# Kernel tuning notes

Hardware: AMD Instinct MI355X
Metric: run time of the kernel (lower is better)

## Reference

```python
import jax, jax.numpy as jnp
import numpy as np

S, B, C = 7, 2, 20
LC, LN = 5.0, 0.5  # lambda_coord, lambda_noobj
CELL = 1.0 / S


def _iou(b1, b2):
    # center (x, y, w, h) boxes, broadcastable [..., 4]
    x1a, y1a = b1[..., 0] - b1[..., 2] / 2, b1[..., 1] - b1[..., 3] / 2
    x2a, y2a = b1[..., 0] + b1[..., 2] / 2, b1[..., 1] + b1[..., 3] / 2
    x1b, y1b = b2[..., 0] - b2[..., 2] / 2, b2[..., 1] - b2[..., 3] / 2
    x2b, y2b = b2[..., 0] + b2[..., 2] / 2, b2[..., 1] + b2[..., 3] / 2
    iw = jnp.maximum(jnp.minimum(x2a, x2b) - jnp.maximum(x1a, x1b), 0.0)
    ih = jnp.maximum(jnp.minimum(y2a, y2b) - jnp.maximum(y1a, y1b), 0.0)
    inter = iw * ih
    union = b1[..., 2] * b1[..., 3] + b2[..., 2] * b2[..., 3] - inter
    return inter / jnp.maximum(union, 1e-10)


def setup_inputs() -> dict:
    key = jax.random.key(0)
    k1, k2, k3 = jax.random.split(key, 3)
    N, T = 16384, 16
    outputs = jax.random.normal(k1, (N, S, S, B * 5 + C), dtype=jnp.float32)
    # normalized xywh, kept strictly inside (0,1) so grid indices are valid
    boxes = jax.random.uniform(k2, (N, T, 4), dtype=jnp.float32, minval=0.01, maxval=0.99)
    labels = jax.random.randint(k3, (N, T), 1, C + 1)  # class labels in 1..C
    return {"outputs": outputs, "boxes": boxes, "labels": labels}


def reference(outputs, boxes, labels):
    N = outputs.shape[0]
    T = boxes.shape[1]
    bbox = outputs[..., : B * 5].reshape(N, S, S, B, 5)
    conf = bbox[..., 4]                         # [N,S,S,B]
    cls_logits = outputs[..., B * 5:]           # [N,S,S,C]
    # decode predicted centers to absolute image coords (as in the original)
    gx = jnp.arange(S, dtype=outputs.dtype)[None, :, None]  # column index
    gy = jnp.arange(S, dtype=outputs.dtype)[:, None, None]  # row index
    px = (bbox[..., 0] + gx) * CELL
    py = (bbox[..., 1] + gy) * CELL
    pred = jnp.stack([px, py, bbox[..., 2], bbox[..., 3]], axis=-1)  # [N,S,S,B,4]

    tx, ty, tw, th = boxes[..., 0], boxes[..., 1], boxes[..., 2], boxes[..., 3]  # [N,T]
    gxi = (tx * S).astype(jnp.int32)
    gyi = (ty * S).astype(jnp.int32)
    offx = tx * S - gxi.astype(tx.dtype)
    offy = ty * S - gyi.astype(ty.dtype)

    bi = jnp.arange(N)[:, None]  # [N,1] broadcasts with [N,T]
    cell_pred = pred[bi, gyi, gxi]          # [N,T,B,4]
    cell_conf = conf[bi, gyi, gxi]          # [N,T,B]
    cell_cls = cls_logits[bi, gyi, gxi]     # [N,T,C]

    ious = _iou(boxes[:, :, None, :], cell_pred)   # [N,T,B]
    best = (B - 1) - jnp.argmax(ious[..., ::-1], axis=-1)  # [N,T]

    bp = jnp.take_along_axis(cell_pred, best[:, :, None, None], axis=2)[:, :, 0, :]  # [N,T,4]
    bconf = jnp.take_along_axis(cell_conf, best[:, :, None], axis=2)[:, :, 0]        # [N,T]

    eps = 1e-6
    box_loss = (
        (bp[..., 0] - offx) ** 2
        + (bp[..., 1] - offy) ** 2
        + (jnp.sqrt(jnp.maximum(bp[..., 2], eps)) - jnp.sqrt(jnp.maximum(tw, eps))) ** 2
        + (jnp.sqrt(jnp.maximum(bp[..., 3], eps)) - jnp.sqrt(jnp.maximum(th, eps))) ** 2
    ).sum(axis=-1)                                     # [N]
    obj_loss = ((bconf - 1.0) ** 2).sum(axis=-1)        # [N]

    probs = jax.nn.softmax(cell_cls, axis=-1)           # [N,T,C]
    onehot = jax.nn.one_hot(labels - 1, C, dtype=probs.dtype)
    class_loss = ((probs - onehot) ** 2).sum(axis=-1).sum(axis=-1)  # [N]

    obj_mask = jnp.zeros((N, S, S, B), dtype=bool).at[bi, gyi, gxi, best].set(True)
    nm = ~obj_mask
    cnt = nm.sum(axis=(1, 2, 3)).astype(conf.dtype)     # always > 0 (T < S*S*B)
    noobj_loss = (conf ** 2 * nm).sum(axis=(1, 2, 3)) / cnt  # mean over unmasked conf

    per_img = LC * box_loss + class_loss + obj_loss + LN * noobj_loss
    return per_img.mean()
```

## Files before the change

kernel.cpp:

```cpp
#include <hip/hip_runtime.h>

#define Cnum 20
#define NCH  30
#define NCONF 98
#define IMGF 1470
#define LCf 5.0f
#define LNf 0.5f

__global__ __launch_bounds__(256) void yolo_loss_kernel(
    const float* __restrict__ outputs,
    const float* __restrict__ boxes,
    const int*   __restrict__ labels,
    float*       __restrict__ per_img)
{
    const int tid  = threadIdx.x;
    const int wave = tid >> 6;
    const int lane = tid & 63;
    const int n    = blockIdx.x * 4 + wave;
    const int t    = lane >> 2;
    const int q    = lane & 3;

    const float* img = outputs + (size_t)n * IMGF;

    const float4 bx = reinterpret_cast<const float4*>(boxes)[(size_t)n * 16 + t];
    const int   lab = labels[(size_t)n * 16 + t] - 1;

    const float tx = bx.x, ty = bx.y, tw = bx.z, th = bx.w;
    const float fx = tx * 7.0f, fy = ty * 7.0f;
    const int gxi = (int)fx, gyi = (int)fy;
    const float offx = fx - (float)gxi;
    const float offy = fy - (float)gyi;
    const int cellIdx = gyi * 7 + gxi;
    const float* cell = img + cellIdx * NCH;

    float ns;
    {
        int c = lane >> 1, b = lane & 1;
        float cf = img[c * NCH + b * 5 + 4];
        ns = cf * cf;
        if (lane < NCONF - 64) {
            int s2 = lane + 64;
            int c2 = s2 >> 1, b2 = s2 & 1;
            float cf2 = img[c2 * NCH + b2 * 5 + 4];
            ns += cf2 * cf2;
        }
    }

    float f[8] = {0.f, 0.f, 0.f, 0.f, 0.f, 0.f, 0.f, 0.f};
    if (q == 0) {
        #pragma unroll
        for (int i = 0; i < 8; ++i) f[i] = cell[i];
    } else if (q == 1) {
        f[0] = cell[8];
        f[1] = cell[9];
    }
    const float e5 = __shfl_xor(f[5], 1);
    const float e6 = __shfl_xor(f[6], 1);
    const float e7 = __shfl_xor(f[7], 1);

    float px = 0.f, py = 0.f, pw = 0.f, ph = 0.f, pc = 0.f, iou_own = 0.f;
    if (q < 2) {
        float rx = (q == 0) ? f[0] : e5;
        float ry = (q == 0) ? f[1] : e6;
        pw       = (q == 0) ? f[2] : e7;
        ph       = (q == 0) ? f[3] : f[0];
        pc       = (q == 0) ? f[4] : f[1];
        px = (rx + (float)gxi) * (1.0f / 7.0f);
        py = (ry + (float)gyi) * (1.0f / 7.0f);

        float x1a = tx - tw * 0.5f, y1a = ty - th * 0.5f;
        float x2a = tx + tw * 0.5f, y2a = ty + th * 0.5f;
        float x1b = px - pw * 0.5f, y1b = py - ph * 0.5f;
        float x2b = px + pw * 0.5f, y2b = py + ph * 0.5f;
        float iw = fmaxf(fminf(x2a, x2b) - fmaxf(x1a, x1b), 0.0f);
        float ih = fmaxf(fminf(y2a, y2b) - fmaxf(y1a, y1b), 0.0f);
        float inter = iw * ih;
        float uni = tw * th + pw * ph - inter;
        iou_own = inter / fmaxf(uni, 1e-10f);
    }
    const float iou_other = __shfl_xor(iou_own, 1);
    int bestq = 0;
    if (q < 2) {
        float i0 = (q == 0) ? iou_own   : iou_other;
        float i1 = (q == 0) ? iou_other : iou_own;
        bestq = (i1 >= i0) ? 1 : 0;
    }
    const int best = __shfl(bestq, lane & ~3);
    const int s = cellIdx * 2 + best;

    float contrib = 0.0f;
    const float eps = 1e-6f;
    if (q == best) {
        float dx = px - offx, dy = py - offy;
        float dw = sqrtf(fmaxf(pw, eps)) - sqrtf(fmaxf(tw, eps));
        float dh = sqrtf(fmaxf(ph, eps)) - sqrtf(fmaxf(th, eps));
        float box_l = dx * dx + dy * dy + dw * dw + dh * dh;
        float obj_l = (pc - 1.0f) * (pc - 1.0f);
        contrib = LCf * box_l + obj_l;
    }

    bool firstv = true;
    #pragma unroll
    for (int j = 0; j < 15; ++j) {
        int sj = __shfl(s, 4 * j);
        if (j < t && sj == s) firstv = false;
    }
    float ms = 0.0f, mc = 0.0f;
    if (q == best && firstv) { ms = pc * pc; mc = 1.0f; }

    {
        float cv[5];
        #pragma unroll
        for (int i = 0; i < 5; ++i) cv[i] = cell[10 + q * 5 + i];
        float m = fmaxf(fmaxf(fmaxf(cv[0], cv[1]), fmaxf(cv[2], cv[3])), cv[4]);
        m = fmaxf(m, __shfl_xor(m, 1));
        m = fmaxf(m, __shfl_xor(m, 2));
        float esum = 0.f, e2 = 0.f, elab = 0.f;
        #pragma unroll
        for (int i = 0; i < 5; ++i) {
            float e = __expf(cv[i] - m);
            esum += e; e2 += e * e;
            if (q * 5 + i == lab) elab = e;
        }
        esum += __shfl_xor(esum, 1);  esum += __shfl_xor(esum, 2);
        e2   += __shfl_xor(e2,   1);  e2   += __shfl_xor(e2,   2);
        elab += __shfl_xor(elab, 1);  elab += __shfl_xor(elab, 2);
        if (q == 0) {
            float inv = 1.0f / esum;
            contrib += e2 * inv * inv - 2.0f * elab * inv + 1.0f;
        }
    }

    #pragma unroll
    for (int off = 32; off > 0; off >>= 1) {
        contrib += __shfl_xor(contrib, off);
        ms      += __shfl_xor(ms,      off);
        mc      += __shfl_xor(mc,      off);
        ns      += __shfl_xor(ns,      off);
    }
    if (lane == 0)
        per_img[n] = contrib + LNf * (ns - ms) / (98.0f - mc);
}

__global__ __launch_bounds__(1024) void reduce_mean_kernel(
    const float* __restrict__ per_img, float* __restrict__ out, int N)
{
    __shared__ double sd[16];
    double acc = 0.0;
    const float4* p4 = reinterpret_cast<const float4*>(per_img);
    for (int i = threadIdx.x; i < N / 4; i += 1024) {
        float4 v = p4[i];
        acc += (double)v.x + (double)v.y + (double)v.z + (double)v.w;
    }
    #pragma unroll
    for (int off = 32; off > 0; off >>= 1) acc += __shfl_xor(acc, off);
    if ((threadIdx.x & 63) == 0) sd[threadIdx.x >> 6] = acc;
    __syncthreads();
    if (threadIdx.x == 0) {
        double t = 0.0;
        #pragma unroll
        for (int w = 0; w < 16; ++w) t += sd[w];
        out[0] = (float)(t / (double)N);
    }
}

extern "C" void kernel_launch(void* const* d_in, const int* in_sizes, int n_in,
                              void* d_out, int out_size, void* d_ws, size_t ws_size,
                              hipStream_t stream) {
    const float* outputs = (const float*)d_in[0];
    const float* boxes   = (const float*)d_in[1];
    const int*   labels  = (const int*)d_in[2];
    float* out = (float*)d_out;

    const int N = in_sizes[0] / IMGF;
    float* per_img = (float*)d_ws;

    yolo_loss_kernel<<<N / 4, 256, 0, stream>>>(outputs, boxes, labels, per_img);
    reduce_mean_kernel<<<1, 1024, 0, stream>>>(per_img, out, N);
}
```

Baseline: 27.87 us.

## Stage each block's four images into LDS via direct global-to-LDS loads

Each 256-thread block now copies its four images' full prediction tensors (about 23.5 KB) into shared memory with 16-byte global_load_lds transfers, synchronises, then reads confidences, box fields and class logits from LDS. The cell box fields are read directly per lane instead of being loaded into registers and exchanged with cross-lane shuffles. The aim is to replace scattered, poorly coalesced global reads with fully contiguous streaming loads, since the strided confidence reads already touch nearly every cache line. In exchange, the large LDS footprint limits how many blocks fit on a CU, and the barrier stops compute from overlapping the loads within a block.

```diff
diff --git a/kernel.cpp b/kernel.cpp
--- a/kernel.cpp
+++ b/kernel.cpp
@@ -4,6 +4,7 @@
 #define NCH  30
 #define NCONF 98
 #define IMGF 1470
+#define IPB  4
 #define LCf 5.0f
 #define LNf 0.5f
 
@@ -16,14 +17,31 @@
     const int tid  = threadIdx.x;
     const int wave = tid >> 6;
     const int lane = tid & 63;
-    const int n    = blockIdx.x * 4 + wave;
+    const int n0   = blockIdx.x * IPB;
+    const int n    = n0 + wave;
     const int t    = lane >> 2;
     const int q    = lane & 3;
 
-    const float* img = outputs + (size_t)n * IMGF;
+    __shared__ float s_all[IPB * IMGF];
+
+    const float* gsrc = outputs + (size_t)n0 * IMGF;
+    #pragma unroll
+    for (int k = 0; k < 6; ++k) {
+        int j = tid + k * 256;
+        if (j < (IPB * IMGF) / 4) {
+            __builtin_amdgcn_global_load_lds(
+                (const __attribute__((address_space(1))) void*)(gsrc + (size_t)j * 4),
+                (__attribute__((address_space(3))) void*)((char*)s_all + (size_t)(k * 256 + wave * 64) * 16),
+                16, 0, 0);
+        }
+    }
 
     const float4 bx = reinterpret_cast<const float4*>(boxes)[(size_t)n * 16 + t];
     const int   lab = labels[(size_t)n * 16 + t] - 1;
+
+    __syncthreads();
+
+    const float* img = s_all + wave * IMGF;
 
     const float tx = bx.x, ty = bx.y, tw = bx.z, th = bx.w;
     const float fx = tx * 7.0f, fy = ty * 7.0f;
@@ -46,25 +64,13 @@
         }
     }
 
-    float f[8] = {0.f, 0.f, 0.f, 0.f, 0.f, 0.f, 0.f, 0.f};
-    if (q == 0) {
-        #pragma unroll
-        for (int i = 0; i < 8; ++i) f[i] = cell[i];
-    } else if (q == 1) {
-        f[0] = cell[8];
-        f[1] = cell[9];
-    }
-    const float e5 = __shfl_xor(f[5], 1);
-    const float e6 = __shfl_xor(f[6], 1);
-    const float e7 = __shfl_xor(f[7], 1);
-
     float px = 0.f, py = 0.f, pw = 0.f, ph = 0.f, pc = 0.f, iou_own = 0.f;
     if (q < 2) {
-        float rx = (q == 0) ? f[0] : e5;
-        float ry = (q == 0) ? f[1] : e6;
-        pw       = (q == 0) ? f[2] : e7;
-        ph       = (q == 0) ? f[3] : f[0];
-        pc       = (q == 0) ? f[4] : f[1];
+        float rx = cell[q * 5 + 0];
+        float ry = cell[q * 5 + 1];
+        pw       = cell[q * 5 + 2];
+        ph       = cell[q * 5 + 3];
+        pc       = cell[q * 5 + 4];
         px = (rx + (float)gxi) * (1.0f / 7.0f);
         py = (ry + (float)gyi) * (1.0f / 7.0f);
 
@@ -175,6 +181,6 @@
     const int N = in_sizes[0] / IMGF;
     float* per_img = (float*)d_ws;
 
-    yolo_loss_kernel<<<N / 4, 256, 0, stream>>>(outputs, boxes, labels, per_img);
+    yolo_loss_kernel<<<N / IPB, 256, 0, stream>>>(outputs, boxes, labels, per_img);
     reduce_mean_kernel<<<1, 1024, 0, stream>>>(per_img, out, N);
 }
```

Measured after the change: 25.84 us. -7.3%, faster.
